# Optimization experiments

Measured on AMD Instinct MI355X. Metric: run time of the kernel, lower is better.

The kernel has to match this reference:

```python
import jax, jax.numpy as jnp
import numpy as np

NUM_HEADS = 6
DIM = 384            # internal attention dim (MultiHeadAttention default)
IN_DIM = 768
HIDDEN = 3072        # int(in_dim * mlp_ratio)
EPS = 1e-5


def _ln(x, w, b):
    m = x.mean(-1, keepdims=True)
    v = ((x - m) ** 2).mean(-1, keepdims=True)
    return (x - m) / jnp.sqrt(v + EPS) * w + b


def _mha(q_in, c_in, Wq, Wkv, Wp, bp):
    # q_in: [b, n, IN_DIM], c_in: [b, m, IN_DIM]
    b, n, _ = q_in.shape
    m = c_in.shape[1]
    h, d = NUM_HEADS, DIM // NUM_HEADS
    scale = d ** -0.5
    q = (q_in @ Wq).reshape(b, n, h, d)
    kv = (c_in @ Wkv).reshape(b, m, 2, h, d)
    k, v = kv[:, :, 0], kv[:, :, 1]
    attn = jax.nn.softmax(jnp.einsum('bnhd,bmhd->bhnm', q, k) * scale, axis=-1)
    out = jnp.einsum('bhnm,bmhd->bnhd', attn, v).reshape(b, n, DIM)
    return out @ Wp + bp


def _mlp(x, W1, b1, W2, b2):
    return jax.nn.gelu(x @ W1 + b1, approximate=False) @ W2 + b2


def setup_inputs() -> dict:
    key = jax.random.key(0)
    ks = jax.random.split(key, 16)
    s = 0.02
    inp = {
        'query': jax.random.normal(ks[0], (8, 1024, IN_DIM), jnp.float32),
        'context': jax.random.normal(ks[1], (8, 2048, IN_DIM), jnp.float32),
        'ln_w': jnp.ones((IN_DIM,), jnp.float32),
        'ln_b': jnp.zeros((IN_DIM,), jnp.float32),
        'a1_wq': jax.random.normal(ks[2], (IN_DIM, DIM), jnp.float32) * s,
        'a1_wkv': jax.random.normal(ks[3], (IN_DIM, 2 * DIM), jnp.float32) * s,
        'a1_wp': jax.random.normal(ks[4], (DIM, IN_DIM), jnp.float32) * s,
        'a1_bp': jnp.zeros((IN_DIM,), jnp.float32),
        'm1_w1': jax.random.normal(ks[5], (IN_DIM, HIDDEN), jnp.float32) * s,
        'm1_b1': jnp.zeros((HIDDEN,), jnp.float32),
        'm1_w2': jax.random.normal(ks[6], (HIDDEN, IN_DIM), jnp.float32) * s,
        'm1_b2': jnp.zeros((IN_DIM,), jnp.float32),
        'a2_wq': jax.random.normal(ks[7], (IN_DIM, DIM), jnp.float32) * s,
        'a2_wkv': jax.random.normal(ks[8], (IN_DIM, 2 * DIM), jnp.float32) * s,
        'a2_wp': jax.random.normal(ks[9], (DIM, IN_DIM), jnp.float32) * s,
        'a2_bp': jnp.zeros((IN_DIM,), jnp.float32),
        'm2_w1': jax.random.normal(ks[10], (IN_DIM, HIDDEN), jnp.float32) * s,
        'm2_b1': jnp.zeros((HIDDEN,), jnp.float32),
        'm2_w2': jax.random.normal(ks[11], (HIDDEN, IN_DIM), jnp.float32) * s,
        'm2_b2': jnp.zeros((IN_DIM,), jnp.float32),
    }
    return inp


def reference(query, context, ln_w, ln_b,
              a1_wq, a1_wkv, a1_wp, a1_bp,
              m1_w1, m1_b1, m1_w2, m1_b2,
              a2_wq, a2_wkv, a2_wp, a2_bp,
              m2_w1, m2_b1, m2_w2, m2_b2):
    q = _ln(query, ln_w, ln_b)                                   # [b, nq, in_dim]
    c = _mha(q, _ln(context, ln_w, ln_b), a1_wq, a1_wkv, a1_wp, a1_bp)  # [b, nq, in_dim]
    c = c + _mlp(_ln(c, ln_w, ln_b), m1_w1, m1_b1, m1_w2, m1_b2)
    c = c + _mha(q, _ln(c, ln_w, ln_b), a2_wq, a2_wkv, a2_wp, a2_bp)
    c = c + _mlp(_ln(c, ln_w, ln_b), m2_w1, m2_b1, m2_w2, m2_b2)
    return (c, q)
```

## Files before the change

kernel.cpp:

```cpp
#include <hip/hip_runtime.h>
#include <hip/hip_bf16.h>
#include <math.h>

typedef unsigned short u16;
typedef __bf16 bf16x8 __attribute__((ext_vector_type(8)));
typedef short s16x4 __attribute__((ext_vector_type(4)));
typedef float f32x4 __attribute__((ext_vector_type(4)));

#define B_   8
#define NQ   1024
#define NC   2048
#define IND  768
#define DIM  384
#define NH   6
#define HD   64
#define HID  3072

__device__ __forceinline__ u16 f2b(float f){
  unsigned int x = __float_as_uint(f);
  return (u16)((x + 0x7fffu + ((x >> 16) & 1u)) >> 16);
}

__device__ __forceinline__ void gl_lds16(const u16* g, u16* l){
  __builtin_amdgcn_global_load_lds(
    (const __attribute__((address_space(1))) unsigned int*)g,
    (__attribute__((address_space(3))) unsigned int*)l, 16, 0, 0);
}

__global__ void wtrans_kernel(const float* __restrict__ W, u16* __restrict__ Wt,
                              int K, int N){
  __shared__ float tile[32][33];
  int n0 = blockIdx.x * 32, k0 = blockIdx.y * 32;
  int tx = threadIdx.x, ty = threadIdx.y;
  #pragma unroll
  for(int i=0;i<4;i++) tile[ty*4+i][tx] = W[(size_t)(k0+ty*4+i)*N + n0 + tx];
  __syncthreads();
  #pragma unroll
  for(int i=0;i<4;i++) Wt[(size_t)(n0+ty*4+i)*K + k0 + tx] = f2b(tile[tx][ty*4+i]);
}

__global__ void vtrans_kernel(const u16* __restrict__ KV, u16* __restrict__ Vt, int M){
  __shared__ u16 t[64][72];
  int bh = blockIdx.y; int b = bh / NH, h = bh % NH;
  int m0 = blockIdx.x * 64;
  int tx = threadIdx.x & 63, ty = threadIdx.x >> 6;
  #pragma unroll
  for(int i=0;i<16;i++){
    int mm = ty*16+i;
    t[mm][tx] = KV[(size_t)(b*M + m0 + mm)*(2*DIM) + DIM + h*HD + tx];
  }
  __syncthreads();
  #pragma unroll
  for(int i=0;i<16;i++){
    int dd = ty*16+i;
    Vt[(size_t)(bh*HD + dd)*M + m0 + tx] = t[tx][dd];
  }
}

template<bool ALSO_F32>
__global__ void ln_kernel(const float* __restrict__ x, const float* __restrict__ w,
                          const float* __restrict__ bia, u16* __restrict__ yb,
                          float* __restrict__ yf){
  int row = blockIdx.x;
  const float* xr = x + (size_t)row * IND;
  int t = threadIdx.x;
  float v[3];
  v[0] = xr[t]; v[1] = xr[t+256]; v[2] = xr[t+512];
  float s  = v[0]+v[1]+v[2];
  float sq = v[0]*v[0]+v[1]*v[1]+v[2]*v[2];
  #pragma unroll
  for(int o=1;o<64;o<<=1){ s += __shfl_xor(s, o, 64); sq += __shfl_xor(sq, o, 64); }
  __shared__ float ss[4], ssq[4];
  int wid = t >> 6;
  if((t&63)==0){ ss[wid]=s; ssq[wid]=sq; }
  __syncthreads();
  s  = ss[0]+ss[1]+ss[2]+ss[3];
  sq = ssq[0]+ssq[1]+ssq[2]+ssq[3];
  float mean = s * (1.0f/IND);
  float var  = sq * (1.0f/IND) - mean*mean;
  float rs   = rsqrtf(var + 1e-5f);
  #pragma unroll
  for(int i=0;i<3;i++){
    int idx = t + i*256;
    float y = (v[i]-mean)*rs*w[idx] + bia[idx];
    yb[(size_t)row*IND + idx] = f2b(y);
    if(ALSO_F32) yf[(size_t)row*IND + idx] = y;
  }
}

template<int TN, int OUTM, bool BIAS, bool GELU_>
__global__ __launch_bounds__(256) void gemm_bt(const u16* __restrict__ A,
    const u16* __restrict__ Wt, const float* __restrict__ bias,
    void* __restrict__ C, int K, int N){
  constexpr int JT = TN / 32;
  __shared__ __align__(16) u16 As[3][128][32];
  __shared__ __align__(16) u16 Bs[3][TN][32];
  int rowblk = blockIdx.x * 128, colblk = blockIdx.y * TN;
  int tid = threadIdx.x;
  int lane = tid & 63, wv = tid >> 6;
  int wm = (wv >> 1) * 64, wn = (wv & 1) * (16*JT);
  int l16 = lane & 15, quad = lane >> 4;
  f32x4 acc[4][JT] = {};
  int sr = lane >> 2;
  int sc = (((lane & 3) ^ ((lane >> 3) & 3)) * 8);
  int rc = ((quad ^ ((l16 >> 1) & 3)) * 8);
  const u16* Ap = A  + (size_t)(rowblk + wv*16 + sr) * K + sc;
  const u16* Bp = Wt + (size_t)(colblk + wv*16 + sr) * K + sc;

  auto stage = [&](int step, int bi){
    int kt = step * 32;
    gl_lds16(Ap + kt,                 &As[bi][wv*16][0]);
    gl_lds16(Ap + (size_t)64*K + kt,  &As[bi][64 + wv*16][0]);
    gl_lds16(Bp + kt,                 &Bs[bi][wv*16][0]);
    if constexpr (TN == 128)
      gl_lds16(Bp + (size_t)64*K + kt, &Bs[bi][64 + wv*16][0]);
  };
  auto compute = [&](int bi){
    bf16x8 af[4], bfr[JT];
    #pragma unroll
    for(int i=0;i<4;i++)  af[i]  = *(const bf16x8*)&As[bi][wm + i*16 + l16][rc];
    #pragma unroll
    for(int j=0;j<JT;j++) bfr[j] = *(const bf16x8*)&Bs[bi][wn + j*16 + l16][rc];
    #pragma unroll
    for(int i=0;i<4;i++)
      #pragma unroll
      for(int j=0;j<JT;j++)
        acc[i][j] = __builtin_amdgcn_mfma_f32_16x16x32_bf16(af[i], bfr[j], acc[i][j], 0, 0, 0);
  };

  int nt = K / 32;
  stage(0, 0); stage(1, 1); stage(2, 2);

  int bi = 0;
  for(int t = 0; t < nt - 3; ++t){
    if constexpr (TN == 128) asm volatile("s_waitcnt vmcnt(8)" ::: "memory");
    else                     asm volatile("s_waitcnt vmcnt(6)" ::: "memory");
    __builtin_amdgcn_s_barrier();
    __builtin_amdgcn_sched_barrier(0);
    compute(bi);
    __builtin_amdgcn_sched_barrier(0);
    asm volatile("" ::: "memory");
    __builtin_amdgcn_s_barrier();
    stage(t + 3, bi);
    bi = (bi == 2) ? 0 : bi + 1;
  }
  if constexpr (TN == 128) asm volatile("s_waitcnt vmcnt(8)" ::: "memory");
  else                     asm volatile("s_waitcnt vmcnt(6)" ::: "memory");
  __builtin_amdgcn_s_barrier();
  __builtin_amdgcn_sched_barrier(0);
  compute(bi); bi = (bi == 2) ? 0 : bi + 1;

  if constexpr (TN == 128) asm volatile("s_waitcnt vmcnt(4)" ::: "memory");
  else                     asm volatile("s_waitcnt vmcnt(3)" ::: "memory");
  __builtin_amdgcn_s_barrier();
  __builtin_amdgcn_sched_barrier(0);
  compute(bi); bi = (bi == 2) ? 0 : bi + 1;

  asm volatile("s_waitcnt vmcnt(0)" ::: "memory");
  __builtin_amdgcn_s_barrier();
  __builtin_amdgcn_sched_barrier(0);
  compute(bi);

  #pragma unroll
  for(int i=0;i<4;i++){
    #pragma unroll
    for(int j=0;j<JT;j++){
      int grow = rowblk + wm + i*16 + quad*4;
      int gcol = colblk + wn + j*16 + l16;
      float bv = BIAS ? bias[gcol] : 0.0f;
      #pragma unroll
      for(int rg=0; rg<4; rg++){
        float vval = acc[i][j][rg] + bv;
        if(GELU_) vval = 0.5f * vval * (1.0f + erff(vval * 0.70710678118f));
        size_t idx = (size_t)(grow + rg) * N + gcol;
        if(OUTM == 0)      ((u16*)C)[idx]   = f2b(vval);
        else if(OUTM == 1) ((float*)C)[idx] = vval;
        else               ((float*)C)[idx] += vval;
      }
    }
  }
}

__global__ __launch_bounds__(256) void attn_kernel(const u16* __restrict__ Q,
    const u16* __restrict__ KV, const u16* __restrict__ Vtg,
    u16* __restrict__ AO, int M){
  __shared__ __align__(16) u16 Ks[128][68];
  __shared__ __align__(16) u16 Vs[64][132];
  int tid = threadIdx.x, lane = tid & 63, wv = tid >> 6;
  int bh = blockIdx.x % (B_*NH);
  int qt = blockIdx.x / (B_*NH);
  int h = bh % NH, b = bh / NH;
  int l16 = lane & 15, quad = lane >> 4;
  const float sc2 = 0.18033688011f;

  s16x4 qf[4];
  const u16* qp = Q + (size_t)(b*NQ + qt*64 + wv*16 + l16) * DIM + h*HD + quad*4;
  #pragma unroll
  for(int s=0;s<4;s++) qf[s] = *(const s16x4*)(qp + s*16);

  f32x4 o[4] = {};
  float lacc = 0.f;

  for(int cb = 0; cb < M; cb += 128){
    __syncthreads();
    #pragma unroll
    for(int it=0; it<4; it++){
      int idx = tid + it*256;
      int row = idx >> 3, c8 = (idx & 7) * 8;
      *(int4*)&Ks[row][c8] =
        *(const int4*)(KV + (size_t)(b*M + cb + row)*(2*DIM) + h*HD + c8);
    }
    #pragma unroll
    for(int it=0; it<4; it++){
      int idx = tid + it*256;
      int dd = idx >> 4, c8 = (idx & 15) * 8;
      *(int4*)&Vs[dd][c8] =
        *(const int4*)(Vtg + (size_t)(bh*HD + dd)*M + cb + c8);
    }
    __syncthreads();

    s16x4 pp[8];
    #pragma unroll
    for(int cc=0; cc<8; cc++){
      f32x4 z = {};
      #pragma unroll
      for(int s=0;s<4;s++){
        s16x4 kf = *(const s16x4*)&Ks[cc*16 + l16][quad*4 + s*16];
        z = __builtin_amdgcn_mfma_f32_16x16x16bf16_1k(kf, qf[s], z, 0,0,0);
      }
      f32x4 p;
      #pragma unroll
      for(int j=0;j<4;j++) p[j] = exp2f(z[j]*sc2);
      lacc += (p[0]+p[1]) + (p[2]+p[3]);
      s16x4 pb;
      #pragma unroll
      for(int j=0;j<4;j++) pb[j] = (short)f2b(p[j]);
      pp[cc] = pb;
    }
    #pragma unroll
    for(int dn=0;dn<4;dn++){
      #pragma unroll
      for(int t=0;t<8;t++){
        s16x4 vf = *(const s16x4*)&Vs[dn*16 + l16][quad*4 + t*16];
        o[dn] = __builtin_amdgcn_mfma_f32_16x16x16bf16_1k(vf, pp[t], o[dn], 0,0,0);
      }
    }
  }

  lacc += __shfl_xor(lacc, 16, 64);
  lacc += __shfl_xor(lacc, 32, 64);
  float rl = 1.0f / lacc;

  u16* aop = AO + (size_t)(b*NQ + qt*64 + wv*16 + l16) * DIM + h*HD + quad*4;
  #pragma unroll
  for(int dn=0;dn<4;dn++){
    s16x4 ob;
    #pragma unroll
    for(int r=0;r<4;r++) ob[r] = (short)f2b(o[dn][r] * rl);
    *(s16x4*)(aop + dn*16) = ob;
  }
}

extern "C" void kernel_launch(void* const* d_in, const int* in_sizes, int n_in,
                              void* d_out, int out_size, void* d_ws, size_t ws_size,
                              hipStream_t stream){
  const float* query   = (const float*)d_in[0];
  const float* context = (const float*)d_in[1];
  const float* ln_w  = (const float*)d_in[2];
  const float* ln_b  = (const float*)d_in[3];
  const float* a1_wq = (const float*)d_in[4];
  const float* a1_wkv= (const float*)d_in[5];
  const float* a1_wp = (const float*)d_in[6];
  const float* a1_bp = (const float*)d_in[7];
  const float* m1_w1 = (const float*)d_in[8];
  const float* m1_b1 = (const float*)d_in[9];
  const float* m1_w2 = (const float*)d_in[10];
  const float* m1_b2 = (const float*)d_in[11];
  const float* a2_wq = (const float*)d_in[12];
  const float* a2_wkv= (const float*)d_in[13];
  const float* a2_wp = (const float*)d_in[14];
  const float* a2_bp = (const float*)d_in[15];
  const float* m2_w1 = (const float*)d_in[16];
  const float* m2_b1 = (const float*)d_in[17];
  const float* m2_w2 = (const float*)d_in[18];
  const float* m2_b2 = (const float*)d_in[19];
  (void)in_sizes; (void)n_in; (void)out_size; (void)ws_size;

  float* c_out = (float*)d_out;
  float* q_out = c_out + (size_t)B_*NQ*IND;

  char* base = (char*)d_ws;
  size_t off = 0;
  auto alloc = [&](size_t elems)->u16*{
    u16* p = (u16*)(base + off);
    off += ((elems*2) + 255) & ~(size_t)255;
    return p;
  };
  u16* wq1t  = alloc((size_t)DIM*IND);
  u16* wkv1t = alloc((size_t)2*DIM*IND);
  u16* wp1t  = alloc((size_t)IND*DIM);
  u16* w11t  = alloc((size_t)HID*IND);
  u16* w21t  = alloc((size_t)IND*HID);
  u16* wq2t  = alloc((size_t)DIM*IND);
  u16* wkv2t = alloc((size_t)2*DIM*IND);
  u16* wp2t  = alloc((size_t)IND*DIM);
  u16* w12t  = alloc((size_t)HID*IND);
  u16* w22t  = alloc((size_t)IND*HID);
  u16* qn_b  = alloc((size_t)B_*NQ*IND);
  u16* cn_b  = alloc((size_t)B_*NC*IND);
  u16* Tb    = alloc((size_t)B_*NQ*IND);
  u16* Qb    = alloc((size_t)B_*NQ*DIM);
  u16* KVb   = alloc((size_t)B_*NC*2*DIM);
  u16* AOb   = alloc((size_t)B_*NQ*DIM);
  u16* Hb    = alloc((size_t)B_*NQ*HID);
  u16* Vtb   = Hb;

  dim3 tb(32,8);
  wtrans_kernel<<<dim3(DIM/32,   IND/32), tb, 0, stream>>>(a1_wq,  wq1t,  IND, DIM);
  wtrans_kernel<<<dim3(2*DIM/32, IND/32), tb, 0, stream>>>(a1_wkv, wkv1t, IND, 2*DIM);
  wtrans_kernel<<<dim3(IND/32,   DIM/32), tb, 0, stream>>>(a1_wp,  wp1t,  DIM, IND);
  wtrans_kernel<<<dim3(HID/32,   IND/32), tb, 0, stream>>>(m1_w1,  w11t,  IND, HID);
  wtrans_kernel<<<dim3(IND/32,   HID/32), tb, 0, stream>>>(m1_w2,  w21t,  HID, IND);
  wtrans_kernel<<<dim3(DIM/32,   IND/32), tb, 0, stream>>>(a2_wq,  wq2t,  IND, DIM);
  wtrans_kernel<<<dim3(2*DIM/32, IND/32), tb, 0, stream>>>(a2_wkv, wkv2t, IND, 2*DIM);
  wtrans_kernel<<<dim3(IND/32,   DIM/32), tb, 0, stream>>>(a2_wp,  wp2t,  DIM, IND);
  wtrans_kernel<<<dim3(HID/32,   IND/32), tb, 0, stream>>>(m2_w1,  w12t,  IND, HID);
  wtrans_kernel<<<dim3(IND/32,   HID/32), tb, 0, stream>>>(m2_w2,  w22t,  HID, IND);

  ln_kernel<true ><<<B_*NQ, 256, 0, stream>>>(query,   ln_w, ln_b, qn_b, q_out);
  ln_kernel<false><<<B_*NC, 256, 0, stream>>>(context, ln_w, ln_b, cn_b, nullptr);

  gemm_bt<64,0,false,false><<<dim3(B_*NQ/128, DIM/64),  256, 0, stream>>>(qn_b, wq1t,  nullptr, Qb,  IND, DIM);
  gemm_bt<128,0,false,false><<<dim3(B_*NC/128, 2*DIM/128), 256, 0, stream>>>(cn_b, wkv1t, nullptr, KVb, IND, 2*DIM);
  vtrans_kernel<<<dim3(NC/64, B_*NH), 256, 0, stream>>>(KVb, Vtb, NC);
  attn_kernel<<<B_*NH*(NQ/64), 256, 0, stream>>>(Qb, KVb, Vtb, AOb, NC);
  gemm_bt<64,1,true,false><<<dim3(B_*NQ/128, IND/64), 256, 0, stream>>>(AOb, wp1t, a1_bp, c_out, DIM, IND);
  ln_kernel<false><<<B_*NQ, 256, 0, stream>>>(c_out, ln_w, ln_b, Tb, nullptr);
  gemm_bt<128,0,true,true ><<<dim3(B_*NQ/128, HID/128), 256, 0, stream>>>(Tb, w11t, m1_b1, Hb, IND, HID);
  gemm_bt<64,2,true,false><<<dim3(B_*NQ/128, IND/64), 256, 0, stream>>>(Hb, w21t, m1_b2, c_out, HID, IND);
  ln_kernel<false><<<B_*NQ, 256, 0, stream>>>(c_out, ln_w, ln_b, Tb, nullptr);
  gemm_bt<64,0,false,false><<<dim3(B_*NQ/128, DIM/64),  256, 0, stream>>>(qn_b, wq2t,  nullptr, Qb,  IND, DIM);
  gemm_bt<64,0,false,false><<<dim3(B_*NQ/128, 2*DIM/64), 256, 0, stream>>>(Tb,   wkv2t, nullptr, KVb, IND, 2*DIM);
  vtrans_kernel<<<dim3(NQ/64, B_*NH), 256, 0, stream>>>(KVb, Vtb, NQ);
  attn_kernel<<<B_*NH*(NQ/64), 256, 0, stream>>>(Qb, KVb, Vtb, AOb, NQ);
  gemm_bt<64,2,true,false><<<dim3(B_*NQ/128, IND/64), 256, 0, stream>>>(AOb, wp2t, a2_bp, c_out, DIM, IND);
  ln_kernel<false><<<B_*NQ, 256, 0, stream>>>(c_out, ln_w, ln_b, Tb, nullptr);
  gemm_bt<128,0,true,true ><<<dim3(B_*NQ/128, HID/128), 256, 0, stream>>>(Tb, w12t, m2_b1, Hb, IND, HID);
  gemm_bt<64,2,true,false><<<dim3(B_*NQ/128, IND/64), 256, 0, stream>>>(Hb, w22t, m2_b2, c_out, HID, IND);
}
```

Measured before the change: 740.6 us.

## Prefetch attention KV tiles into registers and use 16x16x32 MFMA for QK

```diff
diff --git a/kernel.cpp b/kernel.cpp
--- a/kernel.cpp
+++ b/kernel.cpp
@@ -174,6 +174,7 @@
         if(GELU_) vval = 0.5f * vval * (1.0f + erff(vval * 0.70710678118f));
         size_t idx = (size_t)(grow + rg) * N + gcol;
         if(OUTM == 0)      ((u16*)C)[idx]   = f2b(vval);
+        else if(OUTM == 3) ((u16*)C)[idx]   = f2b(vval * 0.125f);
         else if(OUTM == 1) ((float*)C)[idx] = vval;
         else               ((float*)C)[idx] += vval;
       }
@@ -184,66 +185,87 @@
 __global__ __launch_bounds__(256) void attn_kernel(const u16* __restrict__ Q,
     const u16* __restrict__ KV, const u16* __restrict__ Vtg,
     u16* __restrict__ AO, int M){
-  __shared__ __align__(16) u16 Ks[128][68];
+  __shared__ __align__(16) u16 Ks[128][72];
   __shared__ __align__(16) u16 Vs[64][132];
   int tid = threadIdx.x, lane = tid & 63, wv = tid >> 6;
   int bh = blockIdx.x % (B_*NH);
   int qt = blockIdx.x / (B_*NH);
   int h = bh % NH, b = bh / NH;
   int l16 = lane & 15, quad = lane >> 4;
-  const float sc2 = 0.18033688011f;
-
-  s16x4 qf[4];
-  const u16* qp = Q + (size_t)(b*NQ + qt*64 + wv*16 + l16) * DIM + h*HD + quad*4;
-  #pragma unroll
-  for(int s=0;s<4;s++) qf[s] = *(const s16x4*)(qp + s*16);
+
+  bf16x8 qf[2];
+  const u16* qp = Q + (size_t)(b*NQ + qt*64 + wv*16 + l16) * DIM + h*HD + quad*8;
+  qf[0] = *(const bf16x8*)(qp);
+  qf[1] = *(const bf16x8*)(qp + 32);
 
   f32x4 o[4] = {};
   float lacc = 0.f;
-
-  for(int cb = 0; cb < M; cb += 128){
-    __syncthreads();
+  int nt = M / 128;
+
+  int4 kr[4], vr[4];
+  auto load_tile = [&](int cb){
     #pragma unroll
     for(int it=0; it<4; it++){
       int idx = tid + it*256;
       int row = idx >> 3, c8 = (idx & 7) * 8;
-      *(int4*)&Ks[row][c8] =
-        *(const int4*)(KV + (size_t)(b*M + cb + row)*(2*DIM) + h*HD + c8);
+      kr[it] = *(const int4*)(KV + (size_t)(b*M + cb + row)*(2*DIM) + h*HD + c8);
     }
     #pragma unroll
     for(int it=0; it<4; it++){
       int idx = tid + it*256;
       int dd = idx >> 4, c8 = (idx & 15) * 8;
-      *(int4*)&Vs[dd][c8] =
-        *(const int4*)(Vtg + (size_t)(bh*HD + dd)*M + cb + c8);
-    }
-    __syncthreads();
+      vr[it] = *(const int4*)(Vtg + (size_t)(bh*HD + dd)*M + cb + c8);
+    }
+  };
+  auto write_tile = [&](){
+    #pragma unroll
+    for(int it=0; it<4; it++){
+      int idx = tid + it*256;
+      int row = idx >> 3, c8 = (idx & 7) * 8;
+      *(int4*)&Ks[row][c8] = kr[it];
+    }
+    #pragma unroll
+    for(int it=0; it<4; it++){
+      int idx = tid + it*256;
+      int dd = idx >> 4, c8 = (idx & 15) * 8;
+      *(int4*)&Vs[dd][c8] = vr[it];
+    }
+  };
+
+  load_tile(0); write_tile(); __syncthreads();
+
+  for(int t = 0; t < nt; ++t){
+    if(t+1 < nt) load_tile((t+1)*128);
 
     s16x4 pp[8];
     #pragma unroll
     for(int cc=0; cc<8; cc++){
       f32x4 z = {};
       #pragma unroll
-      for(int s=0;s<4;s++){
-        s16x4 kf = *(const s16x4*)&Ks[cc*16 + l16][quad*4 + s*16];
-        z = __builtin_amdgcn_mfma_f32_16x16x16bf16_1k(kf, qf[s], z, 0,0,0);
+      for(int s=0;s<2;s++){
+        bf16x8 kf = *(const bf16x8*)&Ks[cc*16 + l16][quad*8 + s*32];
+        z = __builtin_amdgcn_mfma_f32_16x16x32_bf16(kf, qf[s], z, 0,0,0);
       }
-      f32x4 p;
-      #pragma unroll
-      for(int j=0;j<4;j++) p[j] = exp2f(z[j]*sc2);
-      lacc += (p[0]+p[1]) + (p[2]+p[3]);
+      float p0 = __expf(z[0]), p1 = __expf(z[1]);
+      float p2 = __expf(z[2]), p3 = __expf(z[3]);
+      lacc += (p0+p1) + (p2+p3);
       s16x4 pb;
-      #pragma unroll
-      for(int j=0;j<4;j++) pb[j] = (short)f2b(p[j]);
+      pb[0] = (short)f2b(p0); pb[1] = (short)f2b(p1);
+      pb[2] = (short)f2b(p2); pb[3] = (short)f2b(p3);
       pp[cc] = pb;
     }
     #pragma unroll
     for(int dn=0;dn<4;dn++){
       #pragma unroll
-      for(int t=0;t<8;t++){
-        s16x4 vf = *(const s16x4*)&Vs[dn*16 + l16][quad*4 + t*16];
-        o[dn] = __builtin_amdgcn_mfma_f32_16x16x16bf16_1k(vf, pp[t], o[dn], 0,0,0);
+      for(int tt=0;tt<8;tt++){
+        s16x4 vf = *(const s16x4*)&Vs[dn*16 + l16][quad*4 + tt*16];
+        o[dn] = __builtin_amdgcn_mfma_f32_16x16x16bf16_1k(vf, pp[tt], o[dn], 0,0,0);
       }
+    }
+    if(t+1 < nt){
+      __syncthreads();
+      write_tile();
+      __syncthreads();
     }
   }
 
@@ -330,7 +352,7 @@
   ln_kernel<true ><<<B_*NQ, 256, 0, stream>>>(query,   ln_w, ln_b, qn_b, q_out);
   ln_kernel<false><<<B_*NC, 256, 0, stream>>>(context, ln_w, ln_b, cn_b, nullptr);
 
-  gemm_bt<64,0,false,false><<<dim3(B_*NQ/128, DIM/64),  256, 0, stream>>>(qn_b, wq1t,  nullptr, Qb,  IND, DIM);
+  gemm_bt<64,3,false,false><<<dim3(B_*NQ/128, DIM/64),  256, 0, stream>>>(qn_b, wq1t,  nullptr, Qb,  IND, DIM);
   gemm_bt<128,0,false,false><<<dim3(B_*NC/128, 2*DIM/128), 256, 0, stream>>>(cn_b, wkv1t, nullptr, KVb, IND, 2*DIM);
   vtrans_kernel<<<dim3(NC/64, B_*NH), 256, 0, stream>>>(KVb, Vtb, NC);
   attn_kernel<<<B_*NH*(NQ/64), 256, 0, stream>>>(Qb, KVb, Vtb, AOb, NC);
@@ -339,7 +361,7 @@
   gemm_bt<128,0,true,true ><<<dim3(B_*NQ/128, HID/128), 256, 0, stream>>>(Tb, w11t, m1_b1, Hb, IND, HID);
   gemm_bt<64,2,true,false><<<dim3(B_*NQ/128, IND/64), 256, 0, stream>>>(Hb, w21t, m1_b2, c_out, HID, IND);
   ln_kernel<false><<<B_*NQ, 256, 0, stream>>>(c_out, ln_w, ln_b, Tb, nullptr);
-  gemm_bt<64,0,false,false><<<dim3(B_*NQ/128, DIM/64),  256, 0, stream>>>(qn_b, wq2t,  nullptr, Qb,  IND, DIM);
+  gemm_bt<64,3,false,false><<<dim3(B_*NQ/128, DIM/64),  256, 0, stream>>>(qn_b, wq2t,  nullptr, Qb,  IND, DIM);
   gemm_bt<64,0,false,false><<<dim3(B_*NQ/128, 2*DIM/64), 256, 0, stream>>>(Tb,   wkv2t, nullptr, KVb, IND, 2*DIM);
   vtrans_kernel<<<dim3(NQ/64, B_*NH), 256, 0, stream>>>(KVb, Vtb, NQ);
   attn_kernel<<<B_*NH*(NQ/64), 256, 0, stream>>>(Qb, KVb, Vtb, AOb, NQ);
```

New measurement: 833.7 us. 1.13x slower.
